# Optimization experiments

Hardware: AMD Instinct MI355X
Metric: run time of the kernel (lower is better)

## Reference

```python
import jax, jax.numpy as jnp
import numpy as np

NUM_HEADS = 8
DIM_IN = 512
DIM_OUT = 512


def setup_inputs() -> dict:
    key = jax.random.key(0)
    k1, k2, k3, k4, k5, k6 = jax.random.split(key, 6)
    B, T, J, C = 8, 243, 17, DIM_IN
    H = NUM_HEADS
    x = jax.random.normal(k1, (B, T, J, C), dtype=jnp.float32)
    # external attention map over temporal axis per joint: [B,H,J,T,T]
    att_map = jax.random.uniform(k2, (B, H, J, T, T), dtype=jnp.float32)
    weight = jax.random.uniform(k3, (1,), dtype=jnp.float32)
    # learned params (torch Linear stored here as [in,out] so y = x @ W)
    W_qkv = jax.random.normal(k4, (C, 3 * C), dtype=jnp.float32) * (C ** -0.5)
    W_proj = jax.random.normal(k5, (C, DIM_OUT), dtype=jnp.float32) * (C ** -0.5)
    b_proj = jax.random.normal(k6, (DIM_OUT,), dtype=jnp.float32) * 0.02
    return {"x": x, "att_map": att_map, "weight": weight,
            "W_qkv": W_qkv, "W_proj": W_proj, "b_proj": b_proj}


def reference(x, att_map, weight, W_qkv, W_proj, b_proj):
    B, T, J, C = x.shape
    H = NUM_HEADS
    hd = C // H
    scale = hd ** -0.5
    qkv = (x @ W_qkv).reshape(B, T, J, 3, H, hd)
    # permute(3,0,4,1,2,5) then transpose(2,3) -> [3,B,H,J,T,hd]
    qkv = jnp.transpose(qkv, (3, 0, 4, 2, 1, 5))
    q, k, v = qkv[0], qkv[1], qkv[2]
    attn = jax.nn.softmax(jnp.einsum('bhjtd,bhjsd->bhjts', q, k) * scale, axis=-1)
    attn = weight * attn + (1.0 - weight) * att_map  # dropout is identity (p=0 / eval)
    out = jnp.einsum('bhjts,bhjsd->bhjtd', attn, v)  # [B,H,J,T,hd]
    out = jnp.transpose(out, (0, 3, 2, 1, 4)).reshape(B, T, J, H * hd)
    return out @ W_proj + b_proj
```

## Files before the change

### kernel.cpp

```cpp
#include <hip/hip_runtime.h>
#include <cstddef>
#include <cstdint>

#define NHEADS 8
#define TT 243
#define JJ 17
#define BB 8
#define CC 512
#define HD 64
#define MROWS 33048
#define TJ 4131
#define HJ 136

typedef __attribute__((ext_vector_type(8))) short bf16x8;
typedef __attribute__((ext_vector_type(4))) float f32x4;

__device__ __forceinline__ unsigned short f2bf(float f) {
    unsigned u = __float_as_uint(f);
    unsigned r = (u + 0x7fff + ((u >> 16) & 1)) >> 16;
    return (unsigned short)r;
}
__device__ __forceinline__ float b2f(unsigned short u) {
    return __uint_as_float(((unsigned)u) << 16);
}
__device__ __forceinline__ void async16(const void* g, void* l) {
    __builtin_amdgcn_global_load_lds(
        (const __attribute__((address_space(1))) void*)g,
        (__attribute__((address_space(3))) void*)l, 16, 0, 0);
}

__global__ __launch_bounds__(256) void convert_x(
    const float* __restrict__ in, unsigned short* __restrict__ out, int n4)
{
    for (int i = blockIdx.x * 256 + threadIdx.x; i < n4; i += gridDim.x * 256) {
        const float4 v = *(const float4*)(in + (size_t)i * 4);
        ushort4 o;
        o.x = f2bf(v.x); o.y = f2bf(v.y); o.z = f2bf(v.z); o.w = f2bf(v.w);
        *(ushort4*)(out + (size_t)i * 4) = o;
    }
}

__global__ __launch_bounds__(256) void transpose_w(
    const float* __restrict__ src, unsigned short* __restrict__ dst, int N)
{
    __shared__ unsigned short tile[64][65];
    const int tid = threadIdx.x;
    const int c = tid & 63, r4 = tid >> 6;
    const int n0 = blockIdx.x << 6, k0 = blockIdx.y << 6;
    #pragma unroll
    for (int p = 0; p < 16; ++p) {
        const int r = (p << 2) + r4;
        tile[r][c] = f2bf(src[(size_t)(k0 + r) * N + n0 + c]);
    }
    __syncthreads();
    #pragma unroll
    for (int p = 0; p < 16; ++p) {
        const int rr = (p << 2) + r4;
        dst[(size_t)(n0 + rr) * 512 + k0 + c] = tile[c][rr];
    }
}

__global__ __launch_bounds__(256) void gemm_qkv(
    const unsigned short* __restrict__ xb, const unsigned short* __restrict__ wt,
    unsigned short* __restrict__ qb, unsigned short* __restrict__ kb,
    unsigned short* __restrict__ vb)
{
    __shared__ unsigned short As[128 * 32];
    __shared__ unsigned short Bs[128 * 32];
    __shared__ unsigned short Cq[4][16][72];
    const int tid = threadIdx.x;
    const int wave = tid >> 6, lane = tid & 63;
    const int m0 = blockIdx.y << 7, n0 = blockIdx.x << 7;
    const int wr = wave >> 1, wc = wave & 1;

    f32x4 acc[4][4];
    #pragma unroll
    for (int i = 0; i < 4; ++i)
        #pragma unroll
        for (int j = 0; j < 4; ++j) acc[i][j] = (f32x4){0.f, 0.f, 0.f, 0.f};

    const int srow = lane >> 2;
    const int sbyte = (lane & 3) << 4;
    const int arow0 = (wave << 5) + srow;
    const int arow1 = arow0 + 16;
    const size_t am0 = (size_t)min(m0 + arow0, MROWS - 1);
    const size_t am1 = (size_t)min(m0 + arow1, MROWS - 1);
    const char* xbb = (const char*)xb;
    const char* wtb = (const char*)wt;
    char* Asb = (char*)As;
    char* Bsb = (char*)Bs;

    for (int k0 = 0; k0 < 512; k0 += 32) {
        __syncthreads();
        async16(xbb + (am0 * 512 + k0) * 2 + sbyte, Asb + ((wave << 5) << 6));
        async16(xbb + (am1 * 512 + k0) * 2 + sbyte, Asb + (((wave << 5) + 16) << 6));
        async16(wtb + ((size_t)(n0 + arow0) * 512 + k0) * 2 + sbyte, Bsb + ((wave << 5) << 6));
        async16(wtb + ((size_t)(n0 + arow1) * 512 + k0) * 2 + sbyte, Bsb + (((wave << 5) + 16) << 6));
        __syncthreads();
        bf16x8 af[4], bfr[4];
        #pragma unroll
        for (int i = 0; i < 4; ++i)
            af[i] = *(const bf16x8*)&As[((wr << 6) + (i << 4) + (lane & 15)) * 32 + ((lane >> 4) << 3)];
        #pragma unroll
        for (int j = 0; j < 4; ++j)
            bfr[j] = *(const bf16x8*)&Bs[((wc << 6) + (j << 4) + (lane & 15)) * 32 + ((lane >> 4) << 3)];
        #pragma unroll
        for (int i = 0; i < 4; ++i)
            #pragma unroll
            for (int j = 0; j < 4; ++j)
                acc[i][j] = __builtin_amdgcn_mfma_f32_16x16x32_bf16(af[i], bfr[j], acc[i][j], 0, 0, 0);
    }

    const int nw = n0 + (wc << 6);
    const int which = nw >> 9;
    const int h = (nw >> 6) & 7;
    unsigned short* const dst = which == 0 ? qb : (which == 1 ? kb : vb);
    #pragma unroll
    for (int i = 0; i < 4; ++i) {
        #pragma unroll
        for (int j = 0; j < 4; ++j)
            #pragma unroll
            for (int r = 0; r < 4; ++r)
                Cq[wave][((lane >> 4) << 2) + r][(j << 4) + (lane & 15)] = f2bf(acc[i][j][r]);
        #pragma unroll
        for (int qq = 0; qq < 4; ++qq) {
            const int rr = (qq << 2) + (lane >> 4);
            const int ch = lane & 15;
            const ushort4 val = *(const ushort4*)&Cq[wave][rr][ch << 2];
            const int m = m0 + (wr << 6) + (i << 4) + rr;
            if (m < MROWS) {
                const int b = m / TJ; const int rm = m - b * TJ;
                const int t = rm / JJ; const int jj = rm - t * JJ;
                const size_t base = (((size_t)((b * NHEADS + h) * JJ + jj) * TT + t) << 6) + (ch << 2);
                *(ushort4*)(dst + base) = val;
            }
        }
    }
}

__global__ __launch_bounds__(256) void vtrans(
    const unsigned short* __restrict__ vb, unsigned short* __restrict__ vt)
{
    __shared__ unsigned short TL[64 * 264];
    const int tid = threadIdx.x;
    const int bhj = blockIdx.x;
    const unsigned short* src = vb + (size_t)bhj * TT * HD;

    {
        const int d = tid >> 2, qq = tid & 3;
        *(ushort4*)(TL + d * 264 + 240 + (qq << 2)) = make_ushort4(0, 0, 0, 0);
    }
    __syncthreads();
    #pragma unroll
    for (int p = 0; p < 16; ++p) {
        const int idxq = tid + (p << 8);
        const int t = idxq >> 4;
        if (t < TT) {
            const int d0 = (idxq & 15) << 2;
            const ushort4 u = *(const ushort4*)(src + t * HD + d0);
            TL[(d0 + 0) * 264 + t] = u.x;
            TL[(d0 + 1) * 264 + t] = u.y;
            TL[(d0 + 2) * 264 + t] = u.z;
            TL[(d0 + 3) * 264 + t] = u.w;
        }
    }
    __syncthreads();
    unsigned short* dst = vt + ((size_t)bhj << 14);
    #pragma unroll
    for (int p = 0; p < 8; ++p) {
        const int cw = tid + (p << 8);
        const int d = cw >> 5, c = cw & 31;
        const ushort4 a = *(const ushort4*)(TL + d * 264 + (c << 3));
        const ushort4 bq = *(const ushort4*)(TL + d * 264 + (c << 3) + 4);
        *(ushort4*)(dst + (d << 8) + (c << 3)) = a;
        *(ushort4*)(dst + (d << 8) + (c << 3) + 4) = bq;
    }
}

__global__ __launch_bounds__(256, 4) void attn_mfma(
    const unsigned short* __restrict__ qb, const unsigned short* __restrict__ kb,
    const unsigned short* __restrict__ vt, const float* __restrict__ att,
    const float* __restrict__ wptr, unsigned short* __restrict__ ob)
{
    __shared__ unsigned short ST[64 * 264];

    const int tid = threadIdx.x;
    const int wave = tid >> 6, lane = tid & 63;
    const int tile = blockIdx.x & 3, bhj = blockIdx.x >> 2;
    const int row0 = tile << 6;

    const unsigned short* q = qb + (size_t)bhj * TT * HD;
    const unsigned short* k = kb + (size_t)bhj * TT * HD;
    const float* am = att + (size_t)bhj * TT * TT;
    const float w = wptr[0];

    const int lm = lane & 15, lk = lane >> 4;
    bf16x8 qf[4][2];
    #pragma unroll
    for (int mi = 0; mi < 4; ++mi) {
        const int r = min(row0 + (mi << 4) + lm, TT - 1);
        #pragma unroll
        for (int kb2 = 0; kb2 < 2; ++kb2)
            qf[mi][kb2] = *(const bf16x8*)(q + r * HD + (kb2 << 5) + (lk << 3));
    }
    f32x4 acc[4][4];
    #pragma unroll
    for (int mi = 0; mi < 4; ++mi)
        #pragma unroll
        for (int nj = 0; nj < 4; ++nj) acc[mi][nj] = (f32x4){0.f, 0.f, 0.f, 0.f};
    #pragma unroll
    for (int kb2 = 0; kb2 < 2; ++kb2) {
        bf16x8 kf[4];
        #pragma unroll
        for (int nj = 0; nj < 4; ++nj) {
            const int s = min((wave << 6) + (nj << 4) + lm, TT - 1);
            kf[nj] = *(const bf16x8*)(k + s * HD + (kb2 << 5) + (lk << 3));
        }
        #pragma unroll
        for (int mi = 0; mi < 4; ++mi)
            #pragma unroll
            for (int nj = 0; nj < 4; ++nj)
                acc[mi][nj] = __builtin_amdgcn_mfma_f32_16x16x32_bf16(qf[mi][kb2], kf[nj], acc[mi][nj], 0, 0, 0);
    }
    #pragma unroll
    for (int mi = 0; mi < 4; ++mi)
        #pragma unroll
        for (int nj = 0; nj < 4; ++nj)
            #pragma unroll
            for (int r = 0; r < 4; ++r) {
                const int m = (mi << 4) + (lk << 2) + r;
                const int s = (wave << 6) + (nj << 4) + lm;
                ST[m * 264 + s] = f2bf(acc[mi][nj][r] * 0.125f);
            }
    __syncthreads();

    {
        const int row = tid >> 2, part = tid & 3;
        const int trow = row0 + row;
        unsigned short* strow = ST + row * 264;
        if (trow < TT) {
            const float* amr = am + (size_t)trow * TT;

            float areg[15][4];
            #pragma unroll
            for (int i = 0; i < 15; ++i) {
                const int s0 = (part << 2) + (i << 4);
                areg[i][0] = amr[s0 + 0];
                areg[i][1] = amr[s0 + 1];
                areg[i][2] = amr[s0 + 2];
                areg[i][3] = amr[s0 + 3];
            }
            float at0 = 0.f, at1 = 0.f, at2 = 0.f;
            if (part == 0) { at0 = amr[240]; at1 = amr[241]; at2 = amr[242]; }

            float mx = -1e30f;
            #pragma unroll
            for (int i = 0; i < 15; ++i) {
                const ushort4 u = *(const ushort4*)(strow + (part << 2) + (i << 4));
                mx = fmaxf(fmaxf(fmaxf(fmaxf(mx, b2f(u.x)), b2f(u.y)), b2f(u.z)), b2f(u.w));
            }
            if (part == 0)
                for (int s = 240; s < TT; ++s) mx = fmaxf(mx, b2f(strow[s]));
            mx = fmaxf(mx, __shfl_xor(mx, 1));
            mx = fmaxf(mx, __shfl_xor(mx, 2));
            float l = 0.f;
            #pragma unroll
            for (int i = 0; i < 15; ++i) {
                const int s0 = (part << 2) + (i << 4);
                const ushort4 u = *(const ushort4*)(strow + s0);
                const float e0 = __expf(b2f(u.x) - mx), e1 = __expf(b2f(u.y) - mx);
                const float e2 = __expf(b2f(u.z) - mx), e3 = __expf(b2f(u.w) - mx);
                l += (e0 + e1) + (e2 + e3);
                ushort4 o;
                o.x = f2bf(e0); o.y = f2bf(e1); o.z = f2bf(e2); o.w = f2bf(e3);
                *(ushort4*)(strow + s0) = o;
            }
            if (part == 0)
                for (int s = 240; s < TT; ++s) {
                    const float e = __expf(b2f(strow[s]) - mx);
                    l += e; strow[s] = f2bf(e);
                }
            l += __shfl_xor(l, 1);
            l += __shfl_xor(l, 2);
            const float sw = w / l, aw = 1.f - w;
            #pragma unroll
            for (int i = 0; i < 15; ++i) {
                const int s0 = (part << 2) + (i << 4);
                const ushort4 u = *(const ushort4*)(strow + s0);
                ushort4 o;
                o.x = f2bf(b2f(u.x) * sw + aw * areg[i][0]);
                o.y = f2bf(b2f(u.y) * sw + aw * areg[i][1]);
                o.z = f2bf(b2f(u.z) * sw + aw * areg[i][2]);
                o.w = f2bf(b2f(u.w) * sw + aw * areg[i][3]);
                *(ushort4*)(strow + s0) = o;
            }
            if (part == 0) {
                strow[240] = f2bf(b2f(strow[240]) * sw + aw * at0);
                strow[241] = f2bf(b2f(strow[241]) * sw + aw * at1);
                strow[242] = f2bf(b2f(strow[242]) * sw + aw * at2);
                for (int s = TT; s < 256; ++s) strow[s] = 0;
            }
        } else {
            #pragma unroll
            for (int i = 0; i < 16; ++i)
                *(ushort4*)(strow + (part << 2) + (i << 4)) = make_ushort4(0, 0, 0, 0);
        }
    }
    __syncthreads();

    f32x4 oacc[4];
    #pragma unroll
    for (int nj = 0; nj < 4; ++nj) oacc[nj] = (f32x4){0.f, 0.f, 0.f, 0.f};
    const unsigned short* strow3 = ST + ((wave << 4) + lm) * 264;
    const unsigned short* vtg = vt + ((size_t)bhj << 14);
    #pragma unroll 2
    for (int kb8 = 0; kb8 < 8; ++kb8) {
        const bf16x8 pf = *(const bf16x8*)(strow3 + (kb8 << 5) + (lk << 3));
        #pragma unroll
        for (int nj = 0; nj < 4; ++nj) {
            const int d = (nj << 4) + lm;
            const int chunk = (kb8 << 2) + lk;
            const bf16x8 vf = *(const bf16x8*)(vtg + (d << 8) + (chunk << 3));
            oacc[nj] = __builtin_amdgcn_mfma_f32_16x16x32_bf16(pf, vf, oacc[nj], 0, 0, 0);
        }
    }

    const int b = bhj / HJ;
    const int hj = bhj - b * HJ;
    const int h = hj / JJ;
    const int j = hj - h * JJ;
    #pragma unroll
    for (int r = 0; r < 4; ++r) {
        const int t = row0 + (wave << 4) + (lk << 2) + r;
        if (t < TT) {
            unsigned short* orow = ob + (((size_t)((b * TT + t) * JJ + j)) << 9) + (h << 6);
            #pragma unroll
            for (int nj = 0; nj < 4; ++nj)
                orow[(nj << 4) + lm] = f2bf(oacc[nj][r]);
        }
    }
}

__global__ __launch_bounds__(256) void gemm_proj(
    const unsigned short* __restrict__ obb, const unsigned short* __restrict__ wt,
    const float* __restrict__ bias, float* __restrict__ out)
{
    __shared__ unsigned short As[128 * 32];
    __shared__ unsigned short Bs[128 * 32];
    __shared__ float Cp[4][16][68];
    const int tid = threadIdx.x;
    const int wave = tid >> 6, lane = tid & 63;
    const int m0 = blockIdx.y << 7, n0 = blockIdx.x << 7;
    const int wr = wave >> 1, wc = wave & 1;

    f32x4 acc[4][4];
    #pragma unroll
    for (int i = 0; i < 4; ++i)
        #pragma unroll
        for (int j = 0; j < 4; ++j) acc[i][j] = (f32x4){0.f, 0.f, 0.f, 0.f};

    const int srow = lane >> 2;
    const int sbyte = (lane & 3) << 4;
    const int arow0 = (wave << 5) + srow;
    const int arow1 = arow0 + 16;
    const size_t am0 = (size_t)min(m0 + arow0, MROWS - 1);
    const size_t am1 = (size_t)min(m0 + arow1, MROWS - 1);
    const char* ab = (const char*)obb;
    const char* wtb = (const char*)wt;
    char* Asb = (char*)As;
    char* Bsb = (char*)Bs;

    for (int k0 = 0; k0 < 512; k0 += 32) {
        __syncthreads();
        async16(ab + (am0 * 512 + k0) * 2 + sbyte, Asb + ((wave << 5) << 6));
        async16(ab + (am1 * 512 + k0) * 2 + sbyte, Asb + (((wave << 5) + 16) << 6));
        async16(wtb + ((size_t)(n0 + arow0) * 512 + k0) * 2 + sbyte, Bsb + ((wave << 5) << 6));
        async16(wtb + ((size_t)(n0 + arow1) * 512 + k0) * 2 + sbyte, Bsb + (((wave << 5) + 16) << 6));
        __syncthreads();
        bf16x8 af[4], bfr[4];
        #pragma unroll
        for (int i = 0; i < 4; ++i)
            af[i] = *(const bf16x8*)&As[((wr << 6) + (i << 4) + (lane & 15)) * 32 + ((lane >> 4) << 3)];
        #pragma unroll
        for (int j = 0; j < 4; ++j)
            bfr[j] = *(const bf16x8*)&Bs[((wc << 6) + (j << 4) + (lane & 15)) * 32 + ((lane >> 4) << 3)];
        #pragma unroll
        for (int i = 0; i < 4; ++i)
            #pragma unroll
            for (int j = 0; j < 4; ++j)
                acc[i][j] = __builtin_amdgcn_mfma_f32_16x16x32_bf16(af[i], bfr[j], acc[i][j], 0, 0, 0);
    }

    const int ch0 = lane & 15;
    const float4 bvec = *(const float4*)&bias[n0 + (wc << 6) + (ch0 << 2)];
    #pragma unroll
    for (int i = 0; i < 4; ++i) {
        #pragma unroll
        for (int j = 0; j < 4; ++j)
            #pragma unroll
            for (int r = 0; r < 4; ++r)
                Cp[wave][((lane >> 4) << 2) + r][(j << 4) + (lane & 15)] = acc[i][j][r];
        #pragma unroll
        for (int qq = 0; qq < 4; ++qq) {
            const int rr = (qq << 2) + (lane >> 4);
            const int ch = lane & 15;
            float4 val = *(const float4*)&Cp[wave][rr][ch << 2];
            const int m = m0 + (wr << 6) + (i << 4) + rr;
            if (m < MROWS) {
                val.x += bvec.x; val.y += bvec.y; val.z += bvec.z; val.w += bvec.w;
                *(float4*)(out + (size_t)m * 512 + n0 + (wc << 6) + (ch << 2)) = val;
            }
        }
    }
}

extern "C" void kernel_launch(void* const* d_in, const int* in_sizes, int n_in,
                              void* d_out, int out_size, void* d_ws, size_t ws_size,
                              hipStream_t stream)
{
    const float* x    = (const float*)d_in[0];
    const float* att  = (const float*)d_in[1];
    const float* wgt  = (const float*)d_in[2];
    const float* Wqkv = (const float*)d_in[3];
    const float* Wp   = (const float*)d_in[4];
    const float* bp   = (const float*)d_in[5];
    float* out = (float*)d_out;

    const size_t SZ = (size_t)MROWS * 512;
    unsigned short* xb    = (unsigned short*)d_ws;
    unsigned short* wqkvt = xb + SZ;
    unsigned short* wpt   = wqkvt + (size_t)1536 * 512;
    unsigned short* qb    = wpt + (size_t)512 * 512;
    unsigned short* kb    = qb + SZ;
    unsigned short* vb    = kb + SZ;
    unsigned short* ob    = vb + SZ;
    unsigned short* vtb   = ob + SZ;

    convert_x<<<4096, 256, 0, stream>>>(x, xb, (int)(SZ / 4));
    transpose_w<<<dim3(24, 8), 256, 0, stream>>>(Wqkv, wqkvt, 1536);
    transpose_w<<<dim3(8, 8), 256, 0, stream>>>(Wp, wpt, 512);

    gemm_qkv<<<dim3(12, 259), 256, 0, stream>>>(xb, wqkvt, qb, kb, vb);

    vtrans<<<dim3(1088), 256, 0, stream>>>(vb, vtb);

    attn_mfma<<<dim3(1088 * 4), 256, 0, stream>>>(qb, kb, vtb, att, wgt, ob);

    gemm_proj<<<dim3(4, 259), 256, 0, stream>>>(ob, wpt, bp, out);
}
```

Baseline: 617.9 us.

## Double-buffer LDS tiles in QKV and projection GEMM main loops

Both bf16 MFMA GEMM kernels now keep two LDS buffers per operand. The async copy of the next K-slice is issued before computing on the current one, so global-to-LDS loads can overlap with the MFMA work instead of running strictly before it. The loop is fully unrolled two steps at a time. The epilogue staging arrays are aliased onto the same shared buffer to hold LDS usage at 32 KB. This raises LDS use per block, which may reduce occupancy, and adds code size from the unrolling.

```diff
diff --git a/kernel.cpp b/kernel.cpp
--- a/kernel.cpp
+++ b/kernel.cpp
@@ -65,9 +65,12 @@
     unsigned short* __restrict__ qb, unsigned short* __restrict__ kb,
     unsigned short* __restrict__ vb)
 {
-    __shared__ unsigned short As[128 * 32];
-    __shared__ unsigned short Bs[128 * 32];
-    __shared__ unsigned short Cq[4][16][72];
+    __shared__ __align__(16) char smem[32768];
+    char* const A0 = smem;
+    char* const A1 = smem + 8192;
+    char* const B0 = smem + 16384;
+    char* const B1 = smem + 24576;
+
     const int tid = threadIdx.x;
     const int wave = tid >> 6, lane = tid & 63;
     const int m0 = blockIdx.y << 7, n0 = blockIdx.x << 7;
@@ -87,29 +90,46 @@
     const size_t am1 = (size_t)min(m0 + arow1, MROWS - 1);
     const char* xbb = (const char*)xb;
     const char* wtb = (const char*)wt;
-    char* Asb = (char*)As;
-    char* Bsb = (char*)Bs;
-
-    for (int k0 = 0; k0 < 512; k0 += 32) {
+
+#define STAGEQ(Ad, Bd, k0) do { \
+    async16(xbb + (am0 * 512 + (k0)) * 2 + sbyte, (Ad) + ((wave << 5) << 6)); \
+    async16(xbb + (am1 * 512 + (k0)) * 2 + sbyte, (Ad) + (((wave << 5) + 16) << 6)); \
+    async16(wtb + ((size_t)(n0 + arow0) * 512 + (k0)) * 2 + sbyte, (Bd) + ((wave << 5) << 6)); \
+    async16(wtb + ((size_t)(n0 + arow1) * 512 + (k0)) * 2 + sbyte, (Bd) + (((wave << 5) + 16) << 6)); \
+} while (0)
+
+#define COMPUTEQ(Ap, Bp) do { \
+    bf16x8 af[4], bfr[4]; \
+    _Pragma("unroll") \
+    for (int i = 0; i < 4; ++i) \
+        af[i] = *(const bf16x8*)((const unsigned short*)(Ap) + \
+            ((wr << 6) + (i << 4) + (lane & 15)) * 32 + ((lane >> 4) << 3)); \
+    _Pragma("unroll") \
+    for (int j = 0; j < 4; ++j) \
+        bfr[j] = *(const bf16x8*)((const unsigned short*)(Bp) + \
+            ((wc << 6) + (j << 4) + (lane & 15)) * 32 + ((lane >> 4) << 3)); \
+    _Pragma("unroll") \
+    for (int i = 0; i < 4; ++i) \
+        _Pragma("unroll") \
+        for (int j = 0; j < 4; ++j) \
+            acc[i][j] = __builtin_amdgcn_mfma_f32_16x16x32_bf16(af[i], bfr[j], acc[i][j], 0, 0, 0); \
+} while (0)
+
+    STAGEQ(A0, B0, 0);
+    __syncthreads();
+    #pragma unroll
+    for (int t = 0; t < 16; t += 2) {
+        STAGEQ(A1, B1, (t + 1) << 5);
+        COMPUTEQ(A0, B0);
         __syncthreads();
-        async16(xbb + (am0 * 512 + k0) * 2 + sbyte, Asb + ((wave << 5) << 6));
-        async16(xbb + (am1 * 512 + k0) * 2 + sbyte, Asb + (((wave << 5) + 16) << 6));
-        async16(wtb + ((size_t)(n0 + arow0) * 512 + k0) * 2 + sbyte, Bsb + ((wave << 5) << 6));
-        async16(wtb + ((size_t)(n0 + arow1) * 512 + k0) * 2 + sbyte, Bsb + (((wave << 5) + 16) << 6));
+        if (t + 2 < 16) STAGEQ(A0, B0, (t + 2) << 5);
+        COMPUTEQ(A1, B1);
         __syncthreads();
-        bf16x8 af[4], bfr[4];
-        #pragma unroll
-        for (int i = 0; i < 4; ++i)
-            af[i] = *(const bf16x8*)&As[((wr << 6) + (i << 4) + (lane & 15)) * 32 + ((lane >> 4) << 3)];
-        #pragma unroll
-        for (int j = 0; j < 4; ++j)
-            bfr[j] = *(const bf16x8*)&Bs[((wc << 6) + (j << 4) + (lane & 15)) * 32 + ((lane >> 4) << 3)];
-        #pragma unroll
-        for (int i = 0; i < 4; ++i)
-            #pragma unroll
-            for (int j = 0; j < 4; ++j)
-                acc[i][j] = __builtin_amdgcn_mfma_f32_16x16x32_bf16(af[i], bfr[j], acc[i][j], 0, 0, 0);
-    }
+    }
+#undef STAGEQ
+#undef COMPUTEQ
+
+    unsigned short (*Cq)[16][72] = (unsigned short (*)[16][72])smem;
 
     const int nw = n0 + (wc << 6);
     const int which = nw >> 9;
@@ -345,9 +365,12 @@
     const unsigned short* __restrict__ obb, const unsigned short* __restrict__ wt,
     const float* __restrict__ bias, float* __restrict__ out)
 {
-    __shared__ unsigned short As[128 * 32];
-    __shared__ unsigned short Bs[128 * 32];
-    __shared__ float Cp[4][16][68];
+    __shared__ __align__(16) char smem[32768];
+    char* const A0 = smem;
+    char* const A1 = smem + 8192;
+    char* const B0 = smem + 16384;
+    char* const B1 = smem + 24576;
+
     const int tid = threadIdx.x;
     const int wave = tid >> 6, lane = tid & 63;
     const int m0 = blockIdx.y << 7, n0 = blockIdx.x << 7;
@@ -367,29 +390,46 @@
     const size_t am1 = (size_t)min(m0 + arow1, MROWS - 1);
     const char* ab = (const char*)obb;
     const char* wtb = (const char*)wt;
-    char* Asb = (char*)As;
-    char* Bsb = (char*)Bs;
-
-    for (int k0 = 0; k0 < 512; k0 += 32) {
+
+#define STAGEP(Ad, Bd, k0) do { \
+    async16(ab + (am0 * 512 + (k0)) * 2 + sbyte, (Ad) + ((wave << 5) << 6)); \
+    async16(ab + (am1 * 512 + (k0)) * 2 + sbyte, (Ad) + (((wave << 5) + 16) << 6)); \
+    async16(wtb + ((size_t)(n0 + arow0) * 512 + (k0)) * 2 + sbyte, (Bd) + ((wave << 5) << 6)); \
+    async16(wtb + ((size_t)(n0 + arow1) * 512 + (k0)) * 2 + sbyte, (Bd) + (((wave << 5) + 16) << 6)); \
+} while (0)
+
+#define COMPUTEP(Ap, Bp) do { \
+    bf16x8 af[4], bfr[4]; \
+    _Pragma("unroll") \
+    for (int i = 0; i < 4; ++i) \
+        af[i] = *(const bf16x8*)((const unsigned short*)(Ap) + \
+            ((wr << 6) + (i << 4) + (lane & 15)) * 32 + ((lane >> 4) << 3)); \
+    _Pragma("unroll") \
+    for (int j = 0; j < 4; ++j) \
+        bfr[j] = *(const bf16x8*)((const unsigned short*)(Bp) + \
+            ((wc << 6) + (j << 4) + (lane & 15)) * 32 + ((lane >> 4) << 3)); \
+    _Pragma("unroll") \
+    for (int i = 0; i < 4; ++i) \
+        _Pragma("unroll") \
+        for (int j = 0; j < 4; ++j) \
+            acc[i][j] = __builtin_amdgcn_mfma_f32_16x16x32_bf16(af[i], bfr[j], acc[i][j], 0, 0, 0); \
+} while (0)
+
+    STAGEP(A0, B0, 0);
+    __syncthreads();
+    #pragma unroll
+    for (int t = 0; t < 16; t += 2) {
+        STAGEP(A1, B1, (t + 1) << 5);
+        COMPUTEP(A0, B0);
         __syncthreads();
-        async16(ab + (am0 * 512 + k0) * 2 + sbyte, Asb + ((wave << 5) << 6));
-        async16(ab + (am1 * 512 + k0) * 2 + sbyte, Asb + (((wave << 5) + 16) << 6));
-        async16(wtb + ((size_t)(n0 + arow0) * 512 + k0) * 2 + sbyte, Bsb + ((wave << 5) << 6));
-        async16(wtb + ((size_t)(n0 + arow1) * 512 + k0) * 2 + sbyte, Bsb + (((wave << 5) + 16) << 6));
+        if (t + 2 < 16) STAGEP(A0, B0, (t + 2) << 5);
+        COMPUTEP(A1, B1);
         __syncthreads();
-        bf16x8 af[4], bfr[4];
-        #pragma unroll
-        for (int i = 0; i < 4; ++i)
-            af[i] = *(const bf16x8*)&As[((wr << 6) + (i << 4) + (lane & 15)) * 32 + ((lane >> 4) << 3)];
-        #pragma unroll
-        for (int j = 0; j < 4; ++j)
-            bfr[j] = *(const bf16x8*)&Bs[((wc << 6) + (j << 4) + (lane & 15)) * 32 + ((lane >> 4) << 3)];
-        #pragma unroll
-        for (int i = 0; i < 4; ++i)
-            #pragma unroll
-            for (int j = 0; j < 4; ++j)
-                acc[i][j] = __builtin_amdgcn_mfma_f32_16x16x32_bf16(af[i], bfr[j], acc[i][j], 0, 0, 0);
-    }
+    }
+#undef STAGEP
+#undef COMPUTEP
+
+    float (*Cp)[16][68] = (float (*)[16][68])smem;
 
     const int ch0 = lane & 15;
     const float4 bvec = *(const float4*)&bias[n0 + (wc << 6) + (ch0 << 2)];
```

After: 600.1 us. 1.03x faster.
